# Performance work log

Measured on AMD Instinct MI355X. Metric: run time of the kernel, lower is better.

Reference implementation:

```python
import jax, jax.numpy as jnp
import numpy as np

NUM_LAYERS = 4
EMBED = 1024
HEADS = 16
QKV = 1024
MLP = 4096
EPS_LN = 1e-6


def _layernorm(x, scale, bias):
    m = jnp.mean(x, axis=-1, keepdims=True)
    v = jnp.mean(jnp.square(x - m), axis=-1, keepdims=True)
    return (x - m) * jax.lax.rsqrt(v + EPS_LN) * scale + bias


def setup_inputs() -> dict:
    key = jax.random.key(0)
    ks = jax.random.split(key, 12)
    B, L = 4, 1024
    s = 0.02
    inp = {
        "queries": jax.random.normal(ks[0], (B, L, EMBED), dtype=jnp.float32),
        "Wq": jax.random.normal(ks[1], (NUM_LAYERS, EMBED, QKV), dtype=jnp.float32) * s,
        "bq": jnp.zeros((NUM_LAYERS, QKV), dtype=jnp.float32),
        "Wk": jax.random.normal(ks[2], (NUM_LAYERS, EMBED, QKV), dtype=jnp.float32) * s,
        "bk": jnp.zeros((NUM_LAYERS, QKV), dtype=jnp.float32),
        "Wv": jax.random.normal(ks[3], (NUM_LAYERS, EMBED, QKV), dtype=jnp.float32) * s,
        "bv": jnp.zeros((NUM_LAYERS, QKV), dtype=jnp.float32),
        "Wo": jax.random.normal(ks[4], (NUM_LAYERS, QKV, EMBED), dtype=jnp.float32) * s,
        "bo": jnp.zeros((NUM_LAYERS, EMBED), dtype=jnp.float32),
        "ln1_s": jnp.ones((NUM_LAYERS, EMBED), dtype=jnp.float32),
        "ln1_b": jnp.zeros((NUM_LAYERS, EMBED), dtype=jnp.float32),
        "ln2_s": jnp.ones((NUM_LAYERS, EMBED), dtype=jnp.float32),
        "ln2_b": jnp.zeros((NUM_LAYERS, EMBED), dtype=jnp.float32),
        "W1": jax.random.normal(ks[5], (NUM_LAYERS, EMBED, MLP), dtype=jnp.float32) * s,
        "b1": jnp.zeros((NUM_LAYERS, MLP), dtype=jnp.float32),
        "W2": jax.random.normal(ks[6], (NUM_LAYERS, MLP, EMBED), dtype=jnp.float32) * s,
        "b2": jnp.zeros((NUM_LAYERS, EMBED), dtype=jnp.float32),
    }
    return inp


def _block(x, Wq, bq, Wk, bk, Wv, bv, Wo, bo, ln1_s, ln1_b, ln2_s, ln2_b, W1, b1, W2, b2):
    # post-norm block (pre_norm=False)
    B, L, _ = x.shape
    head_dim = EMBED // HEADS
    q = (x @ Wq + bq).reshape(B, L, HEADS, head_dim)
    k = (x @ Wk + bk).reshape(B, L, HEADS, head_dim)
    v = (x @ Wv + bv).reshape(B, L, HEADS, head_dim)
    q = q / (head_dim ** 0.5)
    attn = jnp.einsum("bqhd,bkhd->bhqk", q, k)
    attn = jax.nn.softmax(attn, axis=-1)
    upd = jnp.einsum("bhqk,bkhd->bqhd", attn, v)  # [B,L,H,hd]
    a = upd.reshape(B, L, QKV) @ Wo + bo
    h = _layernorm(a + x, ln1_s, ln1_b)
    z = jax.nn.relu(h @ W1 + b1) @ W2 + b2
    return _layernorm(z + h, ln2_s, ln2_b)


def reference(queries, Wq, bq, Wk, bk, Wv, bv, Wo, bo, ln1_s, ln1_b, ln2_s, ln2_b, W1, b1, W2, b2):
    x = queries
    for l in range(NUM_LAYERS):
        x = _block(x, Wq[l], bq[l], Wk[l], bk[l], Wv[l], bv[l], Wo[l], bo[l],
                   ln1_s[l], ln1_b[l], ln2_s[l], ln2_b[l], W1[l], b1[l], W2[l], b2[l])
    return x
```

## Files before the change

kernel.cpp:

```cpp
#include <hip/hip_runtime.h>
#include <stdint.h>

typedef __bf16 bf16;
typedef __bf16 bf16x8 __attribute__((ext_vector_type(8)));
typedef float floatx4 __attribute__((ext_vector_type(4)));

#define LOG2E 1.44269504088896340736f

__device__ __forceinline__ void gl2lds16(const bf16* g, bf16* l) {
    __builtin_amdgcn_global_load_lds((__attribute__((address_space(1))) void*)g,
                                     (__attribute__((address_space(3))) void*)l,
                                     16, 0, 0);
}

template<int COLS>
__device__ __forceinline__ int swz(int ch, int r) {
    if constexpr (COLS == 32) return ch ^ ((r >> 1) & 3);
    else                      return ch ^ (r & 7);
}

template<int ROWS, int COLS>
__device__ __forceinline__ void stage_tile_sw(bf16* lds, const bf16* g, int srcStride, int wave, int lane) {
    constexpr int NINST = (ROWS * COLS * 2) / 1024;
    constexpr int ROWB  = COLS * 2;
    #pragma unroll
    for (int u = 0; u < NINST / 4; ++u) {
        int t  = wave + u * 4;
        int ob = t * 1024 + lane * 16;
        int r  = ob / ROWB;
        int ch = (ob % ROWB) >> 4;
        int sc = swz<COLS>(ch, r);
        gl2lds16(g + r * srcStride + sc * 8, lds + t * 512);
    }
}

__device__ __forceinline__ void stage_half_512(bf16* lds, const bf16* g, int srcStride, int wave, int lane) {
    #pragma unroll
    for (int u = 0; u < 2; ++u) {
        int t  = wave + u * 8;
        int ob = t * 1024 + lane * 16;
        int r  = ob >> 7;
        int ch = (ob >> 4) & 7;
        int sc = ch ^ (r & 7);
        gl2lds16(g + r * srcStride + sc * 8, lds + t * 512);
    }
}

template<int RELU, int OUTF, int OUTB>
__device__ __forceinline__ void gemm_core(const bf16* __restrict__ A, const bf16* __restrict__ Bt,
                                          const float* __restrict__ bias, float scale,
                                          float* __restrict__ outf, bf16* __restrict__ outb,
                                          int M, int N, int K, int m0, int n0) {
    __shared__ bf16 As[128 * 32];
    __shared__ bf16 Bs[128 * 32];
    const int tid = threadIdx.x, wave = tid >> 6, lane = tid & 63;
    const int wr = wave >> 1, wc = wave & 1;
    const int quad = lane >> 4, lq = lane & 15;
    const int swa = quad ^ ((lq >> 1) & 3);

    floatx4 acc[4][4] = {};
    const bf16* Ap = A + (size_t)m0 * K;
    const bf16* Bp = Bt + (size_t)n0 * K;

    for (int k0 = 0; k0 < K; k0 += 32) {
        stage_tile_sw<128, 32>(As, Ap + k0, K, wave, lane);
        stage_tile_sw<128, 32>(Bs, Bp + k0, K, wave, lane);
        __syncthreads();
        bf16x8 af[4], bfr[4];
        #pragma unroll
        for (int i = 0; i < 4; i++)
            af[i] = *(const bf16x8*)&As[(wr * 64 + i * 16 + lq) * 32 + swa * 8];
        #pragma unroll
        for (int j = 0; j < 4; j++)
            bfr[j] = *(const bf16x8*)&Bs[(wc * 64 + j * 16 + lq) * 32 + swa * 8];
        #pragma unroll
        for (int i = 0; i < 4; i++)
            #pragma unroll
            for (int j = 0; j < 4; j++)
                acc[i][j] = __builtin_amdgcn_mfma_f32_16x16x32_bf16(af[i], bfr[j], acc[i][j], 0, 0, 0);
        __syncthreads();
    }
    #pragma unroll
    for (int j = 0; j < 4; j++) {
        const int gc = n0 + wc * 64 + j * 16 + lq;
        const float bv = bias[gc];
        #pragma unroll
        for (int i = 0; i < 4; i++) {
            #pragma unroll
            for (int r = 0; r < 4; r++) {
                const int gr = m0 + wr * 64 + i * 16 + quad * 4 + r;
                float v = (acc[i][j][r] + bv) * scale;
                if (RELU) v = fmaxf(v, 0.f);
                if (OUTF) outf[(size_t)gr * N + gc] = v;
                if (OUTB) outb[(size_t)gr * N + gc] = (bf16)v;
            }
        }
    }
}

__global__ __launch_bounds__(512, 2) void gemm_mlp1(const bf16* __restrict__ A, const bf16* __restrict__ Bt,
                                                    const float* __restrict__ bias, bf16* __restrict__ out) {
    __shared__ bf16 As[2][2][128 * 64];
    __shared__ bf16 Bs[2][2][128 * 64];
    const int bid = blockIdx.x;
    const int xcd = bid & 7, j = bid >> 3;
    const int mt = xcd * 2 + (j >> 4), nt = j & 15;
    const int m0 = mt * 256, n0 = nt * 256;
    const int tid = threadIdx.x, wave = tid >> 6, lane = tid & 63;
    const int wr = wave >> 2;
    const int wcn = wave & 3;
    const int bwh = wcn >> 1, bwl = wcn & 1;
    const int quad = lane >> 4, lq = lane & 15;
    constexpr int K = 1024;

    const bf16* Ab0 = A + (size_t)m0 * K;
    const bf16* Ab1 = A + (size_t)(m0 + 128) * K;
    const bf16* Bb0 = Bt + (size_t)n0 * K;
    const bf16* Bb1 = Bt + (size_t)(n0 + 128) * K;

    floatx4 acc[8][4] = {};

    stage_half_512(As[0][0], Ab0, K, wave, lane);
    stage_half_512(As[0][1], Ab1, K, wave, lane);
    stage_half_512(Bs[0][0], Bb0, K, wave, lane);
    stage_half_512(Bs[0][1], Bb1, K, wave, lane);

    for (int kt = 0; kt < 16; ++kt) {
        const int cur = kt & 1, nxt = cur ^ 1;
        const int k1 = (kt + 1) * 64;
        const bool pf = (kt < 15);
        __syncthreads();
        const bf16* Ar = As[cur][wr];
        const bf16* Br = Bs[cur][bwh];
        #pragma unroll
        for (int mh = 0; mh < 2; mh++) {
            bf16x8 af[4][2];
            if (mh == 0 && pf) stage_half_512(As[nxt][0], Ab0 + k1, K, wave, lane);
            #pragma unroll
            for (int i2 = 0; i2 < 4; i2++)
                #pragma unroll
                for (int kk = 0; kk < 2; kk++)
                    af[i2][kk] = *(const bf16x8*)&Ar[(mh * 64 + i2 * 16 + lq) * 64 +
                                                     (((kk * 4 + quad) ^ (lq & 7)) * 8)];
            if (pf) {
                if (mh == 0) stage_half_512(As[nxt][1], Ab1 + k1, K, wave, lane);
                else         stage_half_512(Bs[nxt][1], Bb1 + k1, K, wave, lane);
            }
            #pragma unroll
            for (int nh = 0; nh < 2; nh++) {
                bf16x8 bfr[2][2];
                #pragma unroll
                for (int j2 = 0; j2 < 2; j2++)
                    #pragma unroll
                    for (int kk = 0; kk < 2; kk++)
                        bfr[j2][kk] = *(const bf16x8*)&Br[(bwl * 64 + nh * 32 + j2 * 16 + lq) * 64 +
                                                          (((kk * 4 + quad) ^ (lq & 7)) * 8)];
                if (mh == 0 && nh == 1 && pf) stage_half_512(Bs[nxt][0], Bb0 + k1, K, wave, lane);
                __builtin_amdgcn_s_setprio(1);
                #pragma unroll
                for (int i2 = 0; i2 < 4; i2++)
                    #pragma unroll
                    for (int j2 = 0; j2 < 2; j2++)
                        #pragma unroll
                        for (int kk = 0; kk < 2; kk++)
                            acc[mh * 4 + i2][nh * 2 + j2] =
                                __builtin_amdgcn_mfma_f32_16x16x32_bf16(af[i2][kk], bfr[j2][kk],
                                                                        acc[mh * 4 + i2][nh * 2 + j2], 0, 0, 0);
                __builtin_amdgcn_s_setprio(0);
            }
        }
    }

    #pragma unroll
    for (int j2 = 0; j2 < 4; j2++) {
        const int gc = n0 + bwh * 128 + bwl * 64 + j2 * 16 + lq;
        const float bv = bias[gc];
        #pragma unroll
        for (int i2 = 0; i2 < 8; i2++)
            #pragma unroll
            for (int r = 0; r < 4; r++) {
                const int gr = m0 + wr * 128 + i2 * 16 + quad * 4 + r;
                float v = acc[i2][j2][r] + bv;
                out[(size_t)gr * 4096 + gc] = (bf16)fmaxf(v, 0.f);
            }
    }
}

__global__ __launch_bounds__(256) void gemm_qkv(const bf16* A, const bf16* Wt,
                                                const float* bq, const float* bk, const float* bv,
                                                bf16* out) {
    const int bid = blockIdx.x;
    const int xcd = bid & 7, j = bid >> 3;
    const int mloc = j / 24, r = j % 24;
    const int z = r >> 3, nt = r & 7;
    const int mt = xcd * 4 + mloc;
    const bf16* Bt = Wt + (size_t)z * 1024 * 1024;
    const float* bias = (z == 0) ? bq : (z == 1) ? bk : bv;
    bf16* o = out + (size_t)z * 4096 * 1024;
    const float scale = (z == 0) ? 0.125f * LOG2E : 1.f;
    gemm_core<0, 0, 1>(A, Bt, bias, scale, nullptr, o, 4096, 1024, 1024, mt * 128, nt * 128);
}

__global__ __launch_bounds__(256) void gemm_n1024(const bf16* __restrict__ A, const bf16* __restrict__ Bt,
                                                  const float* __restrict__ bias, float* __restrict__ out,
                                                  int K) {
    __shared__ bf16 As[128 * 64];
    __shared__ bf16 Bs[64 * 64];
    const int bid = blockIdx.x;
    const int xcd = bid & 7, j = bid >> 3;
    const int sk = j >> 6, j2 = j & 63;
    const int mt = xcd * 4 + (j2 >> 4);
    const int nt = j2 & 15;
    const int m0 = mt * 128, n0 = nt * 64;
    const int Kh = K >> 1;
    const int tid = threadIdx.x, wave = tid >> 6, lane = tid & 63;
    const int wr = wave >> 1, wc = wave & 1;
    const int quad = lane >> 4, lq = lane & 15;

    floatx4 acc[4][2] = {};
    const bf16* Ap = A + (size_t)m0 * K + (size_t)sk * Kh;
    const bf16* Bp = Bt + (size_t)n0 * K + (size_t)sk * Kh;

    for (int k0 = 0; k0 < Kh; k0 += 64) {
        stage_tile_sw<128, 64>(As, Ap + k0, K, wave, lane);
        stage_tile_sw<64, 64>(Bs, Bp + k0, K, wave, lane);
        __syncthreads();
        #pragma unroll
        for (int kk = 0; kk < 2; kk++) {
            const int chs = ((kk * 4 + quad) ^ (lq & 7)) * 8;
            bf16x8 af[4], bfr[2];
            #pragma unroll
            for (int i = 0; i < 4; i++)
                af[i] = *(const bf16x8*)&As[(wr * 64 + i * 16 + lq) * 64 + chs];
            #pragma unroll
            for (int jj = 0; jj < 2; jj++)
                bfr[jj] = *(const bf16x8*)&Bs[(wc * 32 + jj * 16 + lq) * 64 + chs];
            #pragma unroll
            for (int i = 0; i < 4; i++)
                #pragma unroll
                for (int jj = 0; jj < 2; jj++)
                    acc[i][jj] = __builtin_amdgcn_mfma_f32_16x16x32_bf16(af[i], bfr[jj], acc[i][jj], 0, 0, 0);
        }
        __syncthreads();
    }
    float* op = out + (size_t)sk * 4194304;
    #pragma unroll
    for (int jj = 0; jj < 2; jj++) {
        const int gc = n0 + wc * 32 + jj * 16 + lq;
        const float bv = sk ? 0.f : bias[gc];
        #pragma unroll
        for (int i = 0; i < 4; i++)
            #pragma unroll
            for (int r = 0; r < 4; r++) {
                const int gr = m0 + wr * 64 + i * 16 + quad * 4 + r;
                op[(size_t)gr * 1024 + gc] = acc[i][jj][r] + bv;
            }
    }
}

__device__ __forceinline__ void ttile(const float* __restrict__ src, bf16* __restrict__ dst,
                                      int K, int N, int n0, int k0) {
    __shared__ float t[32][33];
    const int tx = threadIdx.x & 31, ty = threadIdx.x >> 5;
    #pragma unroll
    for (int i = 0; i < 4; i++)
        t[ty + i * 8][tx] = src[(size_t)(k0 + ty + i * 8) * N + n0 + tx];
    __syncthreads();
    #pragma unroll
    for (int i = 0; i < 4; i++)
        dst[(size_t)(n0 + ty + i * 8) * K + k0 + tx] = (bf16)t[tx][ty + i * 8];
}

__global__ __launch_bounds__(256) void transpose_all(const float* Wq, const float* Wk, const float* Wv,
                                                     const float* Wo, const float* W1, const float* W2,
                                                     bf16* qkvT, bf16* oT, bf16* w1T, bf16* w2T) {
    const int bx = blockIdx.x;
    if (bx < 4096) {
        const int z = bx >> 10, tile = bx & 1023;
        const float* s = (z == 0) ? Wq : (z == 1) ? Wk : (z == 2) ? Wv : Wo;
        bf16* d = (z == 3) ? oT : qkvT + (size_t)z * 1048576;
        ttile(s, d, 1024, 1024, (tile & 31) * 32, (tile >> 5) * 32);
    } else if (bx < 8192) {
        const int tile = bx - 4096;
        ttile(W1, w1T, 1024, 4096, (tile & 127) * 32, (tile >> 7) * 32);
    } else {
        const int tile = bx - 8192;
        ttile(W2, w2T, 4096, 1024, (tile & 31) * 32, (tile >> 5) * 32);
    }
}

__global__ __launch_bounds__(256) void transpose_v(const bf16* v, bf16* vT) {
    __shared__ float t[128][34];
    const int l0 = blockIdx.x * 128, d0 = blockIdx.y * 32, bh = blockIdx.z;
    const int b = bh >> 4, h = bh & 15;
    const int tid = threadIdx.x;
    const int dp = (tid & 15) * 2, lr = tid >> 4;
    #pragma unroll
    for (int i = 0; i < 8; i++) {
        const int lrow = lr + i * 16;
        bf16 two[2];
        *(uint32_t*)two = *(const uint32_t*)&v[(size_t)(b * 1024 + l0 + lrow) * 1024 + h * 64 + d0 + dp];
        t[lrow][dp]     = (float)two[0];
        t[lrow][dp + 1] = (float)two[1];
    }
    __syncthreads();
    #pragma unroll
    for (int u2 = 0; u2 < 2; u2++) {
        const int c = tid + u2 * 256;
        const int d = c >> 4, lp = c & 15;
        bf16 pb[8];
        #pragma unroll
        for (int j = 0; j < 8; j++)
            pb[j] = (bf16)t[j * 16 + lp][d];
        *(bf16x8*)&vT[((size_t)bh * 64 + d0 + d) * 1024 + l0 + lp * 8] = *(bf16x8*)pb;
    }
}

__global__ __launch_bounds__(256) void cvt_f32_bf16(const float* src, bf16* dst) {
    const int i = (blockIdx.x * 256 + threadIdx.x) * 4;
    const float4 v = *(const float4*)(src + i);
    bf16 t4[4] = {(bf16)v.x, (bf16)v.y, (bf16)v.z, (bf16)v.w};
    *(uint64_t*)(dst + i) = *(const uint64_t*)t4;
}

__global__ __launch_bounds__(256) void ln_kernel(const float* __restrict__ a, const float* __restrict__ a2,
                                                 const float* __restrict__ res,
                                                 const float* __restrict__ gamma, const float* __restrict__ beta,
                                                 float* __restrict__ outf, bf16* __restrict__ outb) {
    const int row = blockIdx.x, tid = threadIdx.x;
    const size_t base = (size_t)row * 1024 + tid * 4;
    const float4 av  = *(const float4*)(a + base);
    const float4 a2v = *(const float4*)(a2 + base);
    const float4 rv  = *(const float4*)(res + base);
    float x0 = av.x + a2v.x + rv.x, x1 = av.y + a2v.y + rv.y;
    float x2 = av.z + a2v.z + rv.z, x3 = av.w + a2v.w + rv.w;
    float s  = x0 + x1 + x2 + x3;
    float sq = x0 * x0 + x1 * x1 + x2 * x2 + x3 * x3;
    #pragma unroll
    for (int off = 32; off; off >>= 1) {
        s  += __shfl_xor(s,  off, 64);
        sq += __shfl_xor(sq, off, 64);
    }
    __shared__ float red[8];
    const int wave = tid >> 6, lane = tid & 63;
    if (lane == 0) { red[wave] = s; red[wave + 4] = sq; }
    __syncthreads();
    const float S  = red[0] + red[1] + red[2] + red[3];
    const float SQ = red[4] + red[5] + red[6] + red[7];
    const float mean = S * (1.f / 1024.f);
    const float var  = SQ * (1.f / 1024.f) - mean * mean;
    const float rstd = rsqrtf(var + 1e-6f);
    const int c = tid * 4;
    const float4 g  = *(const float4*)(gamma + c);
    const float4 be = *(const float4*)(beta + c);
    float y0 = (x0 - mean) * rstd * g.x + be.x;
    float y1 = (x1 - mean) * rstd * g.y + be.y;
    float y2 = (x2 - mean) * rstd * g.z + be.z;
    float y3 = (x3 - mean) * rstd * g.w + be.w;
    float4 yo; yo.x = y0; yo.y = y1; yo.z = y2; yo.w = y3;
    *(float4*)(outf + base) = yo;
    bf16 t4[4] = {(bf16)y0, (bf16)y1, (bf16)y2, (bf16)y3};
    *(uint64_t*)(outb + base) = *(const uint64_t*)t4;
}

__global__ __launch_bounds__(256, 2) void attn_kernel(const bf16* __restrict__ Q, const bf16* __restrict__ Kg,
                                                      const bf16* __restrict__ Vt, bf16* __restrict__ O) {
    __shared__ bf16 Ks[128 * 64];
    __shared__ bf16 Vs[64 * 128];
    __shared__ bf16 Ps[128 * 128];
    const int bh = blockIdx.x, qt = blockIdx.y;
    const int b = bh >> 4, h = bh & 15;
    const int tid = threadIdx.x, wave = tid >> 6, lane = tid & 63;
    const int quad = lane >> 4, lq = lane & 15;

    const bf16* qg = Q + ((size_t)b * 1024 + qt * 128) * 1024 + h * 64;
    const bf16* kg = Kg + (size_t)b * 1024 * 1024 + h * 64;
    const bf16* vg = Vt + (size_t)bh * 64 * 1024;

    stage_tile_sw<128, 64>(Ps, qg, 1024, wave, lane);
    __syncthreads();
    bf16x8 aq[2][2];
    #pragma unroll
    for (int i = 0; i < 2; i++)
        #pragma unroll
        for (int kk = 0; kk < 2; kk++) {
            const int row = wave * 32 + i * 16 + lq;
            const int chs = (kk * 4 + quad) ^ (lq & 7);
            aq[i][kk] = *(const bf16x8*)&Ps[row * 64 + chs * 8];
        }

    floatx4 oacc[2][4] = {};
    float lsum[2][4] = {};

    for (int kt = 0; kt < 1024; kt += 128) {
        stage_tile_sw<128, 64>(Ks, kg + (size_t)kt * 1024, 1024, wave, lane);
        stage_tile_sw<64, 128>(Vs, vg + kt, 1024, wave, lane);
        __syncthreads();

        floatx4 sacc[2][8] = {};
        #pragma unroll
        for (int kk = 0; kk < 2; kk++)
            #pragma unroll
            for (int j = 0; j < 8; j++) {
                const int chs = (kk * 4 + quad) ^ (lq & 7);
                bf16x8 bk = *(const bf16x8*)&Ks[(j * 16 + lq) * 64 + chs * 8];
                sacc[0][j] = __builtin_amdgcn_mfma_f32_16x16x32_bf16(aq[0][kk], bk, sacc[0][j], 0, 0, 0);
                sacc[1][j] = __builtin_amdgcn_mfma_f32_16x16x32_bf16(aq[1][kk], bk, sacc[1][j], 0, 0, 0);
            }

        #pragma unroll
        for (int i = 0; i < 2; i++)
            #pragma unroll
            for (int r = 0; r < 4; r++) {
                const int row = wave * 32 + i * 16 + quad * 4 + r;
                float ls = 0.f;
                bf16 pb[8];
                #pragma unroll
                for (int j = 0; j < 8; j++) {
                    const float pv = exp2f(sacc[i][j][r]);
                    ls += pv;
                    pb[j] = (bf16)pv;
                }
                lsum[i][r] += ls;
                *(bf16x8*)&Ps[row * 128 + (lq ^ (row & 7)) * 8] = *(const bf16x8*)pb;
            }

        #pragma unroll
        for (int kk = 0; kk < 4; kk++) {
            bf16x8 ap[2];
            #pragma unroll
            for (int i = 0; i < 2; i++) {
                const int row = wave * 32 + i * 16 + lq;
                const int chs = (kk * 4 + quad) ^ (lq & 7);
                ap[i] = *(const bf16x8*)&Ps[row * 128 + chs * 8];
            }
            #pragma unroll
            for (int dj = 0; dj < 4; dj++) {
                const int chs = (kk * 4 + quad) ^ (lq & 7);
                bf16x8 bv = *(const bf16x8*)&Vs[(dj * 16 + lq) * 128 + chs * 8];
                oacc[0][dj] = __builtin_amdgcn_mfma_f32_16x16x32_bf16(ap[0], bv, oacc[0][dj], 0, 0, 0);
                oacc[1][dj] = __builtin_amdgcn_mfma_f32_16x16x32_bf16(ap[1], bv, oacc[1][dj], 0, 0, 0);
            }
        }
        __syncthreads();
    }

    #pragma unroll
    for (int i = 0; i < 2; i++)
        #pragma unroll
        for (int r = 0; r < 4; r++) {
            float l = lsum[i][r];
            l += __shfl_xor(l, 1, 64); l += __shfl_xor(l, 2, 64);
            l += __shfl_xor(l, 4, 64); l += __shfl_xor(l, 8, 64);
            lsum[i][r] = 1.f / l;
        }
    #pragma unroll
    for (int i = 0; i < 2; i++)
        #pragma unroll
        for (int dj = 0; dj < 4; dj++)
            #pragma unroll
            for (int r = 0; r < 4; r++) {
                const int row = qt * 128 + wave * 32 + i * 16 + quad * 4 + r;
                O[((size_t)b * 1024 + row) * 1024 + h * 64 + dj * 16 + lq] = (bf16)(oacc[i][dj][r] * lsum[i][r]);
            }
}

extern "C" void kernel_launch(void* const* d_in, const int* in_sizes, int n_in,
                              void* d_out, int out_size, void* d_ws, size_t ws_size,
                              hipStream_t stream) {
    const float* queries = (const float*)d_in[0];
    const float* Wq = (const float*)d_in[1];  const float* bq = (const float*)d_in[2];
    const float* Wk = (const float*)d_in[3];  const float* bk = (const float*)d_in[4];
    const float* Wv = (const float*)d_in[5];  const float* bv = (const float*)d_in[6];
    const float* Wo = (const float*)d_in[7];  const float* bo = (const float*)d_in[8];
    const float* ln1_s = (const float*)d_in[9];   const float* ln1_b = (const float*)d_in[10];
    const float* ln2_s = (const float*)d_in[11];  const float* ln2_b = (const float*)d_in[12];
    const float* W1 = (const float*)d_in[13]; const float* b1 = (const float*)d_in[14];
    const float* W2 = (const float*)d_in[15]; const float* b2 = (const float*)d_in[16];

    char* p = (char*)d_ws;
    size_t off = 0;
    auto take = [&](size_t bytes) { void* r = p + off; off += bytes; return r; };
    bf16*  WqkvT = (bf16*)take(6291456);
    bf16*  WoT   = (bf16*)take(2097152);
    bf16*  W1T   = (bf16*)take(8388608);
    bf16*  W2T   = (bf16*)take(8388608);
    bf16*  x_bf  = (bf16*)take(8388608);
    float* xf    = (float*)take(16777216);
    bf16*  qkvb  = (bf16*)take(25165824);
    bf16*  vTb   = (bf16*)take(8388608);
    bf16*  updb  = (bf16*)take(8388608);
    float* az    = (float*)take(33554432);
    float* hf    = (float*)take(16777216);
    bf16*  hbf   = (bf16*)take(8388608);
    bf16*  tmlp  = (bf16*)take(33554432);

    cvt_f32_bf16<<<4096, 256, 0, stream>>>(queries, x_bf);

    for (int l = 0; l < 4; ++l) {
        const size_t w1k = (size_t)l * 1024 * 1024;
        const size_t w4m = (size_t)l * 4096 * 1024;
        transpose_all<<<12288, 256, 0, stream>>>(Wq + w1k, Wk + w1k, Wv + w1k, Wo + w1k,
                                                 W1 + w4m, W2 + w4m, WqkvT, WoT, W1T, W2T);

        gemm_qkv<<<768, 256, 0, stream>>>(x_bf, WqkvT,
                                          bq + l * 1024, bk + l * 1024, bv + l * 1024, qkvb);
        transpose_v<<<dim3(8, 2, 64), 256, 0, stream>>>(qkvb + 2 * 4194304, vTb);
        attn_kernel<<<dim3(64, 8), 256, 0, stream>>>(qkvb, qkvb + 4194304, vTb, updb);
        gemm_n1024<<<1024, 256, 0, stream>>>(updb, WoT, bo + l * 1024, az, 1024);
        ln_kernel<<<4096, 256, 0, stream>>>(az, az + 4194304, (l == 0) ? queries : xf,
                                            ln1_s + l * 1024, ln1_b + l * 1024, hf, hbf);
        gemm_mlp1<<<256, 512, 0, stream>>>(hbf, W1T, b1 + l * 4096, tmlp);
        gemm_n1024<<<1024, 256, 0, stream>>>(tmlp, W2T, b2 + l * 1024, az, 4096);
        ln_kernel<<<4096, 256, 0, stream>>>(az, az + 4194304, hf, ln2_s + l * 1024, ln2_b + l * 1024,
                                            (l == 3) ? (float*)d_out : xf, x_bf);
    }
}
```

Baseline: 1.034 ms.

## Restructure MLP1 GEMM into ping-pong schedule with two-tile-deep prefetch

Rewrites the main loop of the MLP up-projection GEMM into four barrier-separated phases, each doing a small LDS fragment load and then a 4x2 MFMA cluster. Global-to-LDS staging now runs two k-tiles ahead instead of one, with explicit vmcnt waits replacing the per-iteration __syncthreads. The aim is to overlap LDS reads, global loads and MFMA work across the two waves groups sharing a CU and to hide more global latency. This adds many more s_barrier calls per iteration and relies on hand-counted vmcnt values, so a miscount could race or stall.

New measurement: 1.042 ms. About the same (+0.7%).

```diff
diff --git a/kernel.cpp b/kernel.cpp
--- a/kernel.cpp
+++ b/kernel.cpp
@@ -108,67 +108,109 @@
     const int m0 = mt * 256, n0 = nt * 256;
     const int tid = threadIdx.x, wave = tid >> 6, lane = tid & 63;
     const int wr = wave >> 2;
-    const int wcn = wave & 3;
-    const int bwh = wcn >> 1, bwl = wcn & 1;
+    const int bwh = (wave >> 1) & 1, bwl = wave & 1;
     const int quad = lane >> 4, lq = lane & 15;
-    constexpr int K = 1024;
-
-    const bf16* Ab0 = A + (size_t)m0 * K;
-    const bf16* Ab1 = A + (size_t)(m0 + 128) * K;
-    const bf16* Bb0 = Bt + (size_t)n0 * K;
-    const bf16* Bb1 = Bt + (size_t)(n0 + 128) * K;
+    constexpr int K = 1024, NT = 16;
+
+    const bf16* Ah0 = A + (size_t)m0 * K;
+    const bf16* Ah1 = A + (size_t)(m0 + 128) * K;
+    const bf16* Bh0 = Bt + (size_t)n0 * K;
+    const bf16* Bh1 = Bt + (size_t)(n0 + 128) * K;
 
     floatx4 acc[8][4] = {};
 
-    stage_half_512(As[0][0], Ab0, K, wave, lane);
-    stage_half_512(As[0][1], Ab1, K, wave, lane);
-    stage_half_512(Bs[0][0], Bb0, K, wave, lane);
-    stage_half_512(Bs[0][1], Bb1, K, wave, lane);
-
-    for (int kt = 0; kt < 16; ++kt) {
-        const int cur = kt & 1, nxt = cur ^ 1;
-        const int k1 = (kt + 1) * 64;
-        const bool pf = (kt < 15);
-        __syncthreads();
+    stage_half_512(As[0][0], Ah0,      K, wave, lane);
+    stage_half_512(As[0][1], Ah1,      K, wave, lane);
+    stage_half_512(Bs[0][0], Bh0,      K, wave, lane);
+    stage_half_512(Bs[0][1], Bh1,      K, wave, lane);
+    stage_half_512(As[1][0], Ah0 + 64, K, wave, lane);
+    stage_half_512(As[1][1], Ah1 + 64, K, wave, lane);
+    stage_half_512(Bs[1][0], Bh0 + 64, K, wave, lane);
+    asm volatile("s_waitcnt vmcnt(6)" ::: "memory");
+    __builtin_amdgcn_s_barrier();
+
+    for (int t = 0; t < NT; ++t) {
+        const int cur = t & 1, nxt = cur ^ 1;
         const bf16* Ar = As[cur][wr];
         const bf16* Br = Bs[cur][bwh];
-        #pragma unroll
-        for (int mh = 0; mh < 2; mh++) {
-            bf16x8 af[4][2];
-            if (mh == 0 && pf) stage_half_512(As[nxt][0], Ab0 + k1, K, wave, lane);
-            #pragma unroll
-            for (int i2 = 0; i2 < 4; i2++)
+        bf16x8 af[4][2], bfr[2][2][2];
+
+        #pragma unroll
+        for (int i2 = 0; i2 < 4; i2++)
+            #pragma unroll
+            for (int kk = 0; kk < 2; kk++)
+                af[i2][kk] = *(const bf16x8*)&Ar[(i2 * 16 + lq) * 64 + (((kk * 4 + quad) ^ (lq & 7)) * 8)];
+        #pragma unroll
+        for (int j2 = 0; j2 < 2; j2++)
+            #pragma unroll
+            for (int kk = 0; kk < 2; kk++)
+                bfr[0][j2][kk] = *(const bf16x8*)&Br[(bwl * 64 + j2 * 16 + lq) * 64 + (((kk * 4 + quad) ^ (lq & 7)) * 8)];
+        if (t + 1 < NT)
+            stage_half_512(Bs[nxt][1], Bh1 + (t + 1) * 64, K, wave, lane);
+        __builtin_amdgcn_s_barrier();
+        __builtin_amdgcn_s_setprio(1);
+        #pragma unroll
+        for (int i2 = 0; i2 < 4; i2++)
+            #pragma unroll
+            for (int j2 = 0; j2 < 2; j2++)
                 #pragma unroll
                 for (int kk = 0; kk < 2; kk++)
-                    af[i2][kk] = *(const bf16x8*)&Ar[(mh * 64 + i2 * 16 + lq) * 64 +
-                                                     (((kk * 4 + quad) ^ (lq & 7)) * 8)];
-            if (pf) {
-                if (mh == 0) stage_half_512(As[nxt][1], Ab1 + k1, K, wave, lane);
-                else         stage_half_512(Bs[nxt][1], Bb1 + k1, K, wave, lane);
-            }
-            #pragma unroll
-            for (int nh = 0; nh < 2; nh++) {
-                bf16x8 bfr[2][2];
+                    acc[i2][j2] = __builtin_amdgcn_mfma_f32_16x16x32_bf16(af[i2][kk], bfr[0][j2][kk], acc[i2][j2], 0, 0, 0);
+        __builtin_amdgcn_s_setprio(0);
+        __builtin_amdgcn_s_barrier();
+
+        #pragma unroll
+        for (int j2 = 0; j2 < 2; j2++)
+            #pragma unroll
+            for (int kk = 0; kk < 2; kk++)
+                bfr[1][j2][kk] = *(const bf16x8*)&Br[(bwl * 64 + 32 + j2 * 16 + lq) * 64 + (((kk * 4 + quad) ^ (lq & 7)) * 8)];
+        __builtin_amdgcn_s_barrier();
+        __builtin_amdgcn_s_setprio(1);
+        #pragma unroll
+        for (int i2 = 0; i2 < 4; i2++)
+            #pragma unroll
+            for (int j2 = 0; j2 < 2; j2++)
                 #pragma unroll
-                for (int j2 = 0; j2 < 2; j2++)
-                    #pragma unroll
-                    for (int kk = 0; kk < 2; kk++)
-                        bfr[j2][kk] = *(const bf16x8*)&Br[(bwl * 64 + nh * 32 + j2 * 16 + lq) * 64 +
-                                                          (((kk * 4 + quad) ^ (lq & 7)) * 8)];
-                if (mh == 0 && nh == 1 && pf) stage_half_512(Bs[nxt][0], Bb0 + k1, K, wave, lane);
-                __builtin_amdgcn_s_setprio(1);
+                for (int kk = 0; kk < 2; kk++)
+                    acc[i2][2 + j2] = __builtin_amdgcn_mfma_f32_16x16x32_bf16(af[i2][kk], bfr[1][j2][kk], acc[i2][2 + j2], 0, 0, 0);
+        __builtin_amdgcn_s_setprio(0);
+        __builtin_amdgcn_s_barrier();
+
+        #pragma unroll
+        for (int i2 = 0; i2 < 4; i2++)
+            #pragma unroll
+            for (int kk = 0; kk < 2; kk++)
+                af[i2][kk] = *(const bf16x8*)&Ar[((64 + i2 * 16) + lq) * 64 + (((kk * 4 + quad) ^ (lq & 7)) * 8)];
+        __builtin_amdgcn_s_barrier();
+        __builtin_amdgcn_s_setprio(1);
+        #pragma unroll
+        for (int i2 = 0; i2 < 4; i2++)
+            #pragma unroll
+            for (int j2 = 0; j2 < 2; j2++)
                 #pragma unroll
-                for (int i2 = 0; i2 < 4; i2++)
-                    #pragma unroll
-                    for (int j2 = 0; j2 < 2; j2++)
-                        #pragma unroll
-                        for (int kk = 0; kk < 2; kk++)
-                            acc[mh * 4 + i2][nh * 2 + j2] =
-                                __builtin_amdgcn_mfma_f32_16x16x32_bf16(af[i2][kk], bfr[j2][kk],
-                                                                        acc[mh * 4 + i2][nh * 2 + j2], 0, 0, 0);
-                __builtin_amdgcn_s_setprio(0);
-            }
+                for (int kk = 0; kk < 2; kk++)
+                    acc[4 + i2][j2] = __builtin_amdgcn_mfma_f32_16x16x32_bf16(af[i2][kk], bfr[0][j2][kk], acc[4 + i2][j2], 0, 0, 0);
+        __builtin_amdgcn_s_setprio(0);
+        __builtin_amdgcn_s_barrier();
+
+        if (t + 2 < NT) {
+            stage_half_512(As[cur][0], Ah0 + (t + 2) * 64, K, wave, lane);
+            stage_half_512(As[cur][1], Ah1 + (t + 2) * 64, K, wave, lane);
+            stage_half_512(Bs[cur][0], Bh0 + (t + 2) * 64, K, wave, lane);
         }
+        if (t <= NT - 3) asm volatile("s_waitcnt vmcnt(6)" ::: "memory");
+        else             asm volatile("s_waitcnt vmcnt(0)" ::: "memory");
+        __builtin_amdgcn_s_barrier();
+        __builtin_amdgcn_s_setprio(1);
+        #pragma unroll
+        for (int i2 = 0; i2 < 4; i2++)
+            #pragma unroll
+            for (int j2 = 0; j2 < 2; j2++)
+                #pragma unroll
+                for (int kk = 0; kk < 2; kk++)
+                    acc[4 + i2][2 + j2] = __builtin_amdgcn_mfma_f32_16x16x32_bf16(af[i2][kk], bfr[1][j2][kk], acc[4 + i2][2 + j2], 0, 0, 0);
+        __builtin_amdgcn_s_setprio(0);
+        __builtin_amdgcn_s_barrier();
     }
 
     #pragma unroll
```
